# Optimization experiments

Measured on AMD Instinct MI355X. Metric: run time of the kernel, lower is better.

Reference implementation:

```python
import jax, jax.numpy as jnp
import numpy as np

B, D, H, M, N, S = 256, 256, 512, 64, 2048, 3
SHIFTS = (1, 0, -1)  # = range(S//2, -S//2, -1); matches np.roll(eye, s, axis=1) one-hot matrices


def setup_inputs():
    key = jax.random.key(0)
    k = jax.random.split(key, 24)
    f32 = jnp.float32

    def rn(i, shape, scale):
        return jax.random.normal(k[i], shape, f32) * scale

    rh = jax.random.uniform(k[3], (B, N), f32)
    wh = jax.random.uniform(k[4], (B, N), f32)
    sc_ih = 1.0 / np.sqrt(D + M)
    sc_h = 1.0 / np.sqrt(H)
    return dict(
        inp=rn(0, (B, D), 1.0),
        h_tm1=rn(1, (B, H), 0.1),
        c_tm1=rn(2, (B, H), 0.1),
        read_head_tm1=rh / rh.sum(1, keepdims=True),
        write_head_tm1=wh / wh.sum(1, keepdims=True),
        memory=rn(5, (B, N, M), 0.5),
        W_ih=rn(6, (4 * H, D + M), sc_ih), W_hh=rn(7, (4 * H, H), sc_h),
        b_ih=jnp.zeros((4 * H,), f32), b_hh=jnp.zeros((4 * H,), f32),
        W_rk=rn(8, (M, H), sc_h), b_rk=rn(9, (M,), 0.01),
        W_wk=rn(10, (M, H), sc_h), b_wk=rn(11, (M,), 0.01),
        W_rc=rn(12, (3, H), sc_h), b_rc=jnp.zeros((3,), f32),
        W_wc=rn(13, (3, H), sc_h), b_wc=jnp.zeros((3,), f32),
        W_rs=rn(14, (S, H), sc_h), b_rs=jnp.zeros((S,), f32),
        W_ws=rn(15, (S, H), sc_h), b_ws=jnp.zeros((S,), f32),
        W_w=rn(16, (2 * M, H), sc_h), b_w=jnp.zeros((2 * M,), f32),
    )


def _head_params(h, Wk, bk, Wc, bc, Ws, bs):
    kk = jnp.tanh(h @ Wk.T + bk)                     # [B,M] key
    c = h @ Wc.T + bc                                # [B,3]
    beta = jax.nn.relu(c[:, 0:1]) + 1e-4             # focus strength
    g = jax.nn.sigmoid(c[:, 1:2])                    # interpolation gate
    gamma = jax.nn.relu(c[:, 2:3]) + 1.0001          # sharpening power
    s = jax.nn.softmax(h @ Ws.T + bs, axis=1)        # [B,S] shift weights
    return kk, s, beta, g, gamma


def _address(memory, head_tm1, kk, s, beta, g, gamma):
    dot = jnp.einsum('bm,bnm->bn', kk, memory)
    nk = jnp.linalg.norm(kk, axis=1, keepdims=True)  # [B,1]
    nM = jnp.linalg.norm(memory, axis=2)             # [B,N]
    cos = dot / jnp.maximum(nk * nM, 1e-8)
    content = jax.nn.softmax(beta * cos, axis=1)
    inter = g * content + (1.0 - g) * head_tm1       # gated interpolation [B,N]
    # circular shift; identical math to contracting with the one-hot C tensor
    rolled = jnp.stack([jnp.roll(inter, -sh, axis=1) for sh in SHIFTS], axis=1)  # [B,S,N]
    out = jnp.einsum('bsn,bs->bn', rolled, s)
    out = out ** gamma                               # sharpen
    return out / out.sum(1, keepdims=True)


def reference(inp, h_tm1, c_tm1, read_head_tm1, write_head_tm1, memory,
              W_ih, W_hh, b_ih, b_hh, W_rk, b_rk, W_wk, b_wk,
              W_rc, b_rc, W_wc, b_wc, W_rs, b_rs, W_ws, b_ws, W_w, b_w):
    # read addressing uses previous hidden state
    rp = _head_params(h_tm1, W_rk, b_rk, W_rc, b_rc, W_rs, b_rs)
    read_head = _address(memory, read_head_tm1, *rp)
    M_read = jnp.einsum('bn,bnm->bm', read_head, memory)  # [B,M]
    # LSTMCell controller (torch gate order i,f,g,o)
    x = jnp.concatenate([inp, M_read], axis=1)
    z = x @ W_ih.T + b_ih + h_tm1 @ W_hh.T + b_hh
    zi, zf, zg, zo = jnp.split(z, 4, axis=1)
    c_t = jax.nn.sigmoid(zf) * c_tm1 + jax.nn.sigmoid(zi) * jnp.tanh(zg)
    h_t = jax.nn.sigmoid(zo) * jnp.tanh(c_t)
    # write addressing uses new hidden state
    wp = _head_params(h_t, W_wk, b_wk, W_wc, b_wc, W_ws, b_ws)
    write_head = _address(memory, write_head_tm1, *wp)
    wa = h_t @ W_w.T + b_w
    e = jax.nn.sigmoid(wa[:, :M])                    # erase
    a = jnp.tanh(wa[:, M:])                          # add
    ww = write_head[:, :, None]                      # [B,N,1]
    M_out = memory * (1.0 - ww * e[:, None, :]) + ww * a[:, None, :]
    return (h_t, c_t, read_head, write_head, M_out)
```

## Files before the change

kernel.cpp:

```cpp
#include <hip/hip_runtime.h>
#include <hip/hip_bf16.h>

#define Bb 256
#define Hh 512
#define Mm 64
#define Nn 2048

typedef __attribute__((ext_vector_type(8))) short bf16x8;
typedef __attribute__((ext_vector_type(4))) float f32x4;
typedef __attribute__((ext_vector_type(4))) unsigned short u16x4;
typedef __attribute__((ext_vector_type(8))) unsigned short u16x8;

static __device__ __forceinline__ short f2bf(float f) {
    unsigned u = __float_as_uint(f);
    unsigned r = (u + 0x7FFFu + ((u >> 16) & 1u)) >> 16;
    return (short)r;
}
static __device__ __forceinline__ float bf2f(unsigned short u) {
    return __uint_as_float(((unsigned)u) << 16);
}

__global__ __launch_bounds__(256) void convW_headparams_kernel(
    const float* __restrict__ W_ih, const float* __restrict__ W_hh,
    short* __restrict__ Wb,
    const float* __restrict__ h,
    const float* __restrict__ Wk, const float* __restrict__ bk,
    const float* __restrict__ Wc, const float* __restrict__ bc,
    const float* __restrict__ Ws, const float* __restrict__ bs,
    float* __restrict__ kk, float* __restrict__ par)
{
    if (blockIdx.x < 832) {
        unsigned g = blockIdx.x * 256 + threadIdx.x;
        unsigned j = g / 104u;
        unsigned kq = (g - j * 104u) * 8u;
        const float* src = (kq < 320u) ? (W_ih + (size_t)j * 320 + kq)
                                       : (W_hh + (size_t)j * 512 + (kq - 320u));
        float4 a = ((const float4*)src)[0];
        float4 c = ((const float4*)src)[1];
        bf16x8 o;
        o[0] = f2bf(a.x); o[1] = f2bf(a.y); o[2] = f2bf(a.z); o[3] = f2bf(a.w);
        o[4] = f2bf(c.x); o[5] = f2bf(c.y); o[6] = f2bf(c.z); o[7] = f2bf(c.w);
        *(bf16x8*)(Wb + (size_t)j * 832 + kq) = o;
        return;
    }
    int b = blockIdx.x - 832;
    __shared__ float hs[Hh];
    __shared__ float red[6];
    __shared__ float skk[Mm];
    const float* hb = h + (size_t)b * Hh;
    for (int i = threadIdx.x; i < Hh; i += 256) hs[i] = hb[i];
    __syncthreads();
    int m = threadIdx.x >> 2, sub = threadIdx.x & 3;
    {
        const float* w = Wk + (size_t)m * Hh + sub * 128;
        const float* hh = hs + sub * 128;
        float acc = 0.f;
        #pragma unroll 8
        for (int k = 0; k < 128; ++k) acc += hh[k] * w[k];
        acc += __shfl_xor(acc, 1, 64);
        acc += __shfl_xor(acc, 2, 64);
        if (sub == 0) {
            float v = tanhf(acc + bk[m]);
            kk[(size_t)b * Mm + m] = v;
            skk[m] = v;
        }
    }
    if (threadIdx.x < 24) {
        int o = threadIdx.x >> 2, su = threadIdx.x & 3;
        const float* w = ((o < 3) ? (Wc + (size_t)o * Hh) : (Ws + (size_t)(o - 3) * Hh)) + su * 128;
        const float* hh = hs + su * 128;
        float acc = 0.f;
        #pragma unroll 8
        for (int k = 0; k < 128; ++k) acc += hh[k] * w[k];
        acc += __shfl_xor(acc, 1, 64);
        acc += __shfl_xor(acc, 2, 64);
        if (su == 0) red[o] = acc + ((o < 3) ? bc[o] : bs[o - 3]);
    }
    __syncthreads();
    if (threadIdx.x == 0) {
        float beta  = fmaxf(red[0], 0.f) + 1e-4f;
        float g     = 1.f / (1.f + __expf(-red[1]));
        float gamma = fmaxf(red[2], 0.f) + 1.0001f;
        float l0 = red[3], l1 = red[4], l2 = red[5];
        float mx = fmaxf(l0, fmaxf(l1, l2));
        float e0 = __expf(l0 - mx), e1 = __expf(l1 - mx), e2 = __expf(l2 - mx);
        float inv = 1.f / (e0 + e1 + e2);
        float ssq = 0.f;
        #pragma unroll
        for (int i = 0; i < Mm; ++i) ssq += skk[i] * skk[i];
        float* p = par + (size_t)b * 8;
        p[0] = beta; p[1] = g; p[2] = gamma;
        p[3] = e0 * inv; p[4] = e1 * inv; p[5] = e2 * inv;
        p[6] = sqrtf(ssq);
    }
}

__global__ __launch_bounds__(256) void convM_cos_kernel(
    const float* __restrict__ mem, const float* __restrict__ kk,
    const float* __restrict__ par, float* __restrict__ cosv,
    short* __restrict__ memb)
{
    int b  = blockIdx.x >> 3;
    int n0 = (blockIdx.x & 7) << 8;
    int w  = threadIdx.x >> 6;
    int l  = threadIdx.x & 63;
    int m4 = l & 15;
    int rq = l >> 4;

    float4 kv = ((const float4*)(kk + (size_t)b * Mm))[m4];
    float kn = par[(size_t)b * 8 + 6];
    const f32x4* mb4 = (const f32x4*)(mem + (size_t)b * Nn * Mm);
    short* ob = memb + (size_t)b * Nn * Mm;

    #pragma unroll
    for (int q = 0; q < 16; ++q) {
        int n = n0 + w * 64 + q * 4 + rq;
        f32x4 v = __builtin_nontemporal_load(mb4 + (size_t)n * 16 + m4);
        u16x4 o;
        o[0] = (unsigned short)f2bf(v[0]); o[1] = (unsigned short)f2bf(v[1]);
        o[2] = (unsigned short)f2bf(v[2]); o[3] = (unsigned short)f2bf(v[3]);
        *(u16x4*)(ob + (size_t)n * 64 + m4 * 4) = o;
        float dot = v[0] * kv.x + v[1] * kv.y + v[2] * kv.z + v[3] * kv.w;
        float ss  = v[0] * v[0] + v[1] * v[1] + v[2] * v[2] + v[3] * v[3];
        dot += __shfl_xor(dot, 1, 64); ss += __shfl_xor(ss, 1, 64);
        dot += __shfl_xor(dot, 2, 64); ss += __shfl_xor(ss, 2, 64);
        dot += __shfl_xor(dot, 4, 64); ss += __shfl_xor(ss, 4, 64);
        dot += __shfl_xor(dot, 8, 64); ss += __shfl_xor(ss, 8, 64);
        if (m4 == 0) cosv[(size_t)b * Nn + n] = dot / fmaxf(kn * sqrtf(ss), 1e-8f);
    }
}

__global__ __launch_bounds__(1024) void raddr_mread_convA_kernel(
    const float* __restrict__ cosv, const float* __restrict__ par,
    const float* __restrict__ prev, const short* __restrict__ memb,
    const float* __restrict__ inp, const float* __restrict__ h,
    float* __restrict__ outh, short* __restrict__ Ab)
{
    int b = blockIdx.x;
    int t = threadIdx.x;
    int w = t >> 6, l = t & 63;
    __shared__ float csh[Nn];
    __shared__ float redw[16];
    __shared__ float redM[128][8][8];
    __shared__ float mrdL[Mm];

    const float* pv = par + (size_t)b * 8;
    float beta = pv[0], g = pv[1], gamma = pv[2];
    float s0 = pv[3], s1 = pv[4], s2 = pv[5];

    float v0 = beta * cosv[(size_t)b * Nn + t];
    float v1 = beta * cosv[(size_t)b * Nn + t + 1024];
    float mx = fmaxf(v0, v1);
    #pragma unroll
    for (int msk = 1; msk < 64; msk <<= 1) mx = fmaxf(mx, __shfl_xor(mx, msk, 64));
    if (l == 0) redw[w] = mx;
    __syncthreads();
    mx = redw[0];
    #pragma unroll
    for (int i = 1; i < 16; ++i) mx = fmaxf(mx, redw[i]);
    float e0 = __expf(v0 - mx), e1 = __expf(v1 - mx);
    float sum = e0 + e1;
    #pragma unroll
    for (int msk = 1; msk < 64; msk <<= 1) sum += __shfl_xor(sum, msk, 64);
    __syncthreads();
    if (l == 0) redw[w] = sum;
    __syncthreads();
    sum = 0.f;
    #pragma unroll
    for (int i = 0; i < 16; ++i) sum += redw[i];
    float invs = 1.f / sum;
    const float* pb = prev + (size_t)b * Nn;
    float i0 = g * e0 * invs + (1.f - g) * pb[t];
    float i1 = g * e1 * invs + (1.f - g) * pb[t + 1024];
    csh[t] = i0; csh[t + 1024] = i1;
    __syncthreads();
    int n1 = t + 1024;
    float c0 = s0 * csh[(t + 1) & (Nn - 1)] + s1 * i0 + s2 * csh[(t - 1) & (Nn - 1)];
    float c1 = s0 * csh[(n1 + 1) & (Nn - 1)] + s1 * i1 + s2 * csh[(n1 - 1) & (Nn - 1)];
    float p0 = exp2f(gamma * __log2f(c0));
    float p1 = exp2f(gamma * __log2f(c1));
    float osum = p0 + p1;
    #pragma unroll
    for (int msk = 1; msk < 64; msk <<= 1) osum += __shfl_xor(osum, msk, 64);
    __syncthreads();
// ... 24 lines not shown
    }
    #pragma unroll
    for (int j = 0; j < 8; ++j) redM[r][m8][j] = acc[j];
    __syncthreads();
    #pragma unroll
    for (int s = 64; s >= 1; s >>= 1) {
        if (r < s) {
            #pragma unroll
            for (int j = 0; j < 8; ++j) redM[r][m8][j] += redM[r + s][m8][j];
        }
        __syncthreads();
    }
    if (t < 8) {
        #pragma unroll
        for (int j = 0; j < 8; ++j) mrdL[t * 8 + j] = redM[0][t][j];
    }
    __syncthreads();

    if (t < 104) {
        int kq = t * 8;
        float v[8];
        if (kq < 256) {
            const float* s = inp + (size_t)b * 256 + kq;
            #pragma unroll
            for (int i = 0; i < 8; ++i) v[i] = s[i];
        } else if (kq < 320) {
            #pragma unroll
            for (int i = 0; i < 8; ++i) v[i] = mrdL[kq - 256 + i];
        } else {
            const float* s = h + (size_t)b * 512 + (kq - 320);
            #pragma unroll
            for (int i = 0; i < 8; ++i) v[i] = s[i];
        }
        bf16x8 o;
        #pragma unroll
        for (int i = 0; i < 8; ++i) o[i] = f2bf(v[i]);
        *(bf16x8*)(Ab + (size_t)b * 832 + kq) = o;
    }
}

__global__ __launch_bounds__(256) void lstm_gemm_mfma(
    const short* __restrict__ Ab, const short* __restrict__ Wb,
    const float* __restrict__ b_ih, const float* __restrict__ b_hh,
    float* __restrict__ z)
{
    int t = threadIdx.x;
    int r0 = blockIdx.x * 64, c0 = blockIdx.y * 64;
    int w = t >> 6, l = t & 63;
    int wr = (w >> 1) * 32, wc = (w & 1) * 32;
    int lr = l & 15, kb = (l >> 4) * 8;

    const short* A0 = Ab + (size_t)(r0 + wr + lr) * 832 + kb;
    const short* A1 = A0 + 16 * 832;
    const short* B0 = Wb + (size_t)(c0 + wc + lr) * 832 + kb;
    const short* B1 = B0 + 16 * 832;

    f32x4 acc00 = {0.f, 0.f, 0.f, 0.f}, acc01 = {0.f, 0.f, 0.f, 0.f};
    f32x4 acc10 = {0.f, 0.f, 0.f, 0.f}, acc11 = {0.f, 0.f, 0.f, 0.f};

    #pragma unroll 2
    for (int kt = 0; kt < 26; ++kt) {
        int k0 = kt * 32;
        bf16x8 a0 = *(const bf16x8*)(A0 + k0);
        bf16x8 a1 = *(const bf16x8*)(A1 + k0);
        bf16x8 b0 = *(const bf16x8*)(B0 + k0);
        bf16x8 b1 = *(const bf16x8*)(B1 + k0);
        acc00 = __builtin_amdgcn_mfma_f32_16x16x32_bf16(a0, b0, acc00, 0, 0, 0);
        acc01 = __builtin_amdgcn_mfma_f32_16x16x32_bf16(a0, b1, acc01, 0, 0, 0);
        acc10 = __builtin_amdgcn_mfma_f32_16x16x32_bf16(a1, b0, acc10, 0, 0, 0);
        acc11 = __builtin_amdgcn_mfma_f32_16x16x32_bf16(a1, b1, acc11, 0, 0, 0);
    }
    int rq = (l >> 4) * 4;
    #pragma unroll
    for (int q = 0; q < 4; ++q) {
        int row0 = r0 + wr + rq + q;
        int col0 = c0 + wc + lr;
        z[(size_t)row0 * 2048 + col0] = acc00[q] + b_ih[col0] + b_hh[col0];
        z[(size_t)row0 * 2048 + col0 + 16] = acc01[q] + b_ih[col0 + 16] + b_hh[col0 + 16];
        z[(size_t)(row0 + 16) * 2048 + col0] = acc10[q] + b_ih[col0] + b_hh[col0];
        z[(size_t)(row0 + 16) * 2048 + col0 + 16] = acc11[q] + b_ih[col0 + 16] + b_hh[col0 + 16];
    }
}

__global__ __launch_bounds__(1024) void gates_wparams_kernel(
    const float* __restrict__ z, const float* __restrict__ c_tm1,
    const float* __restrict__ Wk, const float* __restrict__ bk,
    const float* __restrict__ Wc, const float* __restrict__ bc,
    const float* __restrict__ Ws, const float* __restrict__ bs,
    const float* __restrict__ W_w, const float* __restrict__ b_w,
    float* __restrict__ h_out, float* __restrict__ c_out,
    float* __restrict__ kk, float* __restrict__ par, float* __restrict__ ea)
{
    int b = blockIdx.x;
    int t = threadIdx.x;
    __shared__ float hs[Hh];
    __shared__ float red6[6];
    __shared__ float skk[Mm];

    if (t < 512) {
        const float* zb = z + (size_t)b * 2048;
        float zi = zb[t], zf = zb[512 + t], zg = zb[1024 + t], zo = zb[1536 + t];
        float si = 1.f / (1.f + __expf(-zi));
        float sf = 1.f / (1.f + __expf(-zf));
        float so = 1.f / (1.f + __expf(-zo));
        float ct = sf * c_tm1[(size_t)b * 512 + t] + si * tanhf(zg);
        float ht = so * tanhf(ct);
        c_out[(size_t)b * 512 + t] = ct;
        h_out[(size_t)b * 512 + t] = ht;
        hs[t] = ht;
    }
    __syncthreads();

    if (t < 256) {
        int m = t >> 2, sub = t & 3;
        const float* w = Wk + (size_t)m * Hh + sub * 128;
        const float* hh = hs + sub * 128;
        float acc = 0.f;
        #pragma unroll 8
        for (int k = 0; k < 128; ++k) acc += hh[k] * w[k];
        acc += __shfl_xor(acc, 1, 64);
        acc += __shfl_xor(acc, 2, 64);
        if (sub == 0) {
            float v = tanhf(acc + bk[m]);
            skk[m] = v;
            kk[(size_t)b * Mm + m] = v;
        }
    } else if (t < 280) {
        int o = (t - 256) >> 2, su = t & 3;
        const float* w = ((o < 3) ? (Wc + (size_t)o * Hh) : (Ws + (size_t)(o - 3) * Hh)) + su * 128;
        const float* hh = hs + su * 128;
        float acc = 0.f;
        #pragma unroll 8
        for (int k = 0; k < 128; ++k) acc += hh[k] * w[k];
        acc += __shfl_xor(acc, 1, 64);
        acc += __shfl_xor(acc, 2, 64);
        if (su == 0) red6[o] = acc + ((o < 3) ? bc[o] : bs[o - 3]);
    } else if (t >= 512) {
        int o = (t - 512) >> 2, su = t & 3;
        const float* w = W_w + (size_t)o * Hh + su * 128;
        const float* hh = hs + su * 128;
        float acc = 0.f;
        #pragma unroll 8
        for (int k = 0; k < 128; ++k) acc += hh[k] * w[k];
        acc += __shfl_xor(acc, 1, 64);
        acc += __shfl_xor(acc, 2, 64);
        if (su == 0) {
            float v = acc + b_w[o];
            ea[(size_t)b * 128 + o] = (o < Mm) ? (1.f / (1.f + __expf(-v))) : tanhf(v);
        }
    }
    __syncthreads();
    if (t < 64) {
        float v = skk[t];
        float ssq = v * v;
        #pragma unroll
        for (int msk = 1; msk < 64; msk <<= 1) ssq += __shfl_xor(ssq, msk, 64);
        if (t == 0) {
            float beta  = fmaxf(red6[0], 0.f) + 1e-4f;
            float g     = 1.f / (1.f + __expf(-red6[1]));
            float gamma = fmaxf(red6[2], 0.f) + 1.0001f;
            float l0 = red6[3], l1 = red6[4], l2 = red6[5];
            float mx = fmaxf(l0, fmaxf(l1, l2));
            float e0 = __expf(l0 - mx), e1 = __expf(l1 - mx), e2 = __expf(l2 - mx);
            float inv = 1.f / (e0 + e1 + e2);
            float* p = par + (size_t)b * 8;
            p[0] = beta; p[1] = g; p[2] = gamma;
            p[3] = e0 * inv; p[4] = e1 * inv; p[5] = e2 * inv;
            p[6] = sqrtf(ssq);
        }
    }
}

__global__ __launch_bounds__(1024) void wfused_kernel(
    const short* __restrict__ memb, const float* __restrict__ kk,
    const float* __restrict__ par, const float* __restrict__ prev,
    float* __restrict__ outh)
{
    int b = blockIdx.x;
    int t = threadIdx.x;
    int w = t >> 6, l = t & 63;
    __shared__ float csh[Nn];
    __shared__ float redw[16];

    const float* pv = par + (size_t)b * 8;
    float kn = pv[6];
    float beta = pv[0], g = pv[1], gamma = pv[2];
    float s0 = pv[3], s1 = pv[4], s2 = pv[5];

    int m8 = l & 7, rg = l >> 3;
    float kv[8];
    {
        const float* kp = kk + (size_t)b * Mm + m8 * 8;
        #pragma unroll
        for (int j = 0; j < 8; ++j) kv[j] = kp[j];
    }
    const short* mb = memb + (size_t)b * Nn * Mm;
    #pragma unroll 4
    for (int it = 0; it < 16; ++it) {
        int n = it * 128 + w * 8 + rg;
        u16x8 uv = *(const u16x8*)(mb + (size_t)n * 64 + m8 * 8);
        float dot = 0.f, ss = 0.f;
        #pragma unroll
        for (int j = 0; j < 8; ++j) {
            float x = bf2f(uv[j]);
            dot += x * kv[j];
            ss  += x * x;
        }
        dot += __shfl_xor(dot, 1, 64); ss += __shfl_xor(ss, 1, 64);
        dot += __shfl_xor(dot, 2, 64); ss += __shfl_xor(ss, 2, 64);
        dot += __shfl_xor(dot, 4, 64); ss += __shfl_xor(ss, 4, 64);
        if (m8 == 0) csh[n] = dot / fmaxf(kn * sqrtf(ss), 1e-8f);
    }
    __syncthreads();

    float v0 = beta * csh[t], v1 = beta * csh[t + 1024];
    float mx = fmaxf(v0, v1);
    #pragma unroll
    for (int msk = 1; msk < 64; msk <<= 1) mx = fmaxf(mx, __shfl_xor(mx, msk, 64));
    if (l == 0) redw[w] = mx;
    __syncthreads();
    mx = redw[0];
    #pragma unroll
    for (int i = 1; i < 16; ++i) mx = fmaxf(mx, redw[i]);
    float e0 = __expf(v0 - mx), e1 = __expf(v1 - mx);
    float sum = e0 + e1;
    #pragma unroll
    for (int msk = 1; msk < 64; msk <<= 1) sum += __shfl_xor(sum, msk, 64);
    __syncthreads();
    if (l == 0) redw[w] = sum;
    __syncthreads();
    sum = 0.f;
    #pragma unroll
    for (int i = 0; i < 16; ++i) sum += redw[i];
    float invs = 1.f / sum;
    const float* pb = prev + (size_t)b * Nn;
    float i0 = g * e0 * invs + (1.f - g) * pb[t];
    float i1 = g * e1 * invs + (1.f - g) * pb[t + 1024];
    __syncthreads();
    csh[t] = i0; csh[t + 1024] = i1;
    __syncthreads();
    int n1 = t + 1024;
    float c0 = s0 * csh[(t + 1) & (Nn - 1)] + s1 * i0 + s2 * csh[(t - 1) & (Nn - 1)];
    float c1 = s0 * csh[(n1 + 1) & (Nn - 1)] + s1 * i1 + s2 * csh[(n1 - 1) & (Nn - 1)];
    float p0 = exp2f(gamma * __log2f(c0));
    float p1 = exp2f(gamma * __log2f(c1));
    float osum = p0 + p1;
    #pragma unroll
    for (int msk = 1; msk < 64; msk <<= 1) osum += __shfl_xor(osum, msk, 64);
    __syncthreads();
    if (l == 0) redw[w] = osum;
    __syncthreads();
    osum = 0.f;
    #pragma unroll
    for (int i = 0; i < 16; ++i) osum += redw[i];
    float inv2 = 1.f / osum;
    outh[(size_t)b * Nn + t] = p0 * inv2;
    outh[(size_t)b * Nn + n1] = p1 * inv2;
}

template <int BF16SRC>
__global__ __launch_bounds__(256) void mout_kernel(
    const float* __restrict__ mem, const short* __restrict__ memb,
    const float* __restrict__ head, const float* __restrict__ ea,
    float* __restrict__ out)
{
    const size_t total8 = (size_t)Bb * Nn * Mm / 8;
    for (size_t i8 = (size_t)blockIdx.x * 256 + threadIdx.x; i8 < total8;
         i8 += (size_t)2048 * 256) {
        size_t row = i8 >> 3;
        int m8 = (int)(i8 & 7);
        int b = (int)(row >> 11);
        float w = head[row];
        float x[8];
        if (BF16SRC) {
            u16x8 uv = __builtin_nontemporal_load((const u16x8*)memb + i8);
            #pragma unroll
            for (int j = 0; j < 8; ++j) x[j] = bf2f(uv[j]);
        } else {
            f32x4 lo = __builtin_nontemporal_load((const f32x4*)mem + i8 * 2);
            f32x4 hi = __builtin_nontemporal_load((const f32x4*)mem + i8 * 2 + 1);
            #pragma unroll
            for (int j = 0; j < 4; ++j) { x[j] = lo[j]; x[4 + j] = hi[j]; }
        }
        const float* ep = ea + (size_t)b * 128 + m8 * 8;
        const float* ap = ep + 64;
        f32x4 o0, o1;
        #pragma unroll
        for (int j = 0; j < 4; ++j) {
            o0[j] = x[j] * (1.f - w * ep[j]) + w * ap[j];
            o1[j] = x[4 + j] * (1.f - w * ep[4 + j]) + w * ap[4 + j];
        }
        __builtin_nontemporal_store(o0, (f32x4*)out + i8 * 2);
        __builtin_nontemporal_store(o1, (f32x4*)out + i8 * 2 + 1);
    }
}

extern "C" void kernel_launch(void* const* d_in, const int* in_sizes, int n_in,
                              void* d_out, int out_size, void* d_ws, size_t ws_size,
                              hipStream_t stream)
{
    const float* inp   = (const float*)d_in[0];
    const float* h_tm1 = (const float*)d_in[1];
    const float* c_tm1 = (const float*)d_in[2];
    const float* rh0   = (const float*)d_in[3];
    const float* wh0   = (const float*)d_in[4];
    const float* mem   = (const float*)d_in[5];
    const float* W_ih  = (const float*)d_in[6];
    const float* W_hh  = (const float*)d_in[7];
    const float* b_ih  = (const float*)d_in[8];
    const float* b_hh  = (const float*)d_in[9];
    const float* W_rk  = (const float*)d_in[10];
    const float* b_rk  = (const float*)d_in[11];
    const float* W_wk  = (const float*)d_in[12];
    const float* b_wk  = (const float*)d_in[13];
    const float* W_rc  = (const float*)d_in[14];
    const float* b_rc  = (const float*)d_in[15];
    const float* W_wc  = (const float*)d_in[16];
    const float* b_wc  = (const float*)d_in[17];
    const float* W_rs  = (const float*)d_in[18];
    const float* b_rs  = (const float*)d_in[19];
    const float* W_ws  = (const float*)d_in[20];
    const float* b_ws  = (const float*)d_in[21];
    const float* W_w   = (const float*)d_in[22];
    const float* b_w   = (const float*)d_in[23];

    float* out   = (float*)d_out;
    float* h_t   = out;
    float* c_t   = out + 131072;
    float* rhead = out + 262144;
    float* whead = out + 786432;
    float* mo    = out + 1310720;
    float* cosbuf = mo;
    float* zbuf   = mo + 524288;
    short* Ab     = (short*)(mo + 1048576);
    short* Wb     = (short*)(mo + 1179648);

    float* ws  = (float*)d_ws;
    float* kk  = ws;
    float* par = ws + 16384;
    float* ea  = ws + 18432;

    const size_t memb_elems = (size_t)Bb * Nn * Mm;
    const bool big_ws = ws_size >= (size_t)51200 * 4 + memb_elems * 2;
    short* memb = big_ws ? (short*)(ws + 51200)
                         : (short*)(mo + 2097152);

    convW_headparams_kernel<<<1088, 256, 0, stream>>>(
        W_ih, W_hh, Wb, h_tm1, W_rk, b_rk, W_rc, b_rc, W_rs, b_rs, kk, par);
    convM_cos_kernel<<<2048, 256, 0, stream>>>(mem, kk, par, cosbuf, memb);
    raddr_mread_convA_kernel<<<Bb, 1024, 0, stream>>>(
        cosbuf, par, rh0, memb, inp, h_tm1, rhead, Ab);
    lstm_gemm_mfma<<<dim3(4, 32), 256, 0, stream>>>(Ab, Wb, b_ih, b_hh, zbuf);
    gates_wparams_kernel<<<Bb, 1024, 0, stream>>>(
        zbuf, c_tm1, W_wk, b_wk, W_wc, b_wc, W_ws, b_ws, W_w, b_w,
        h_t, c_t, kk, par, ea);
    wfused_kernel<<<Bb, 1024, 0, stream>>>(memb, kk, par, wh0, whead);
    if (big_ws)
        mout_kernel<1><<<2048, 256, 0, stream>>>(mem, memb, whead, ea, mo);
    else
        mout_kernel<0><<<2048, 256, 0, stream>>>(mem, memb, whead, ea, mo);
}
```

Measured before the change: 155.6 us.

## Fuse all NTM stages into one cooperative persistent kernel with grid syncs

Replaces the seven-kernel launch sequence with a single cooperative kernel of 256 blocks of 1024 threads, one block per batch row. Stages are separated by three grid.sync calls, and per-batch data (cosine scores, heads, head parameters) stays in shared memory instead of round-tripping through global buffers. This removes launch overhead and intermediate writes. In exchange, the heavy memory-streaming phases now run with only 256 blocks, the LSTM GEMM uses just one block per tile, and the grid barriers add cost. If the cooperative launch fails, the code falls back to the old multi-kernel path.

```diff
diff --git a/kernel.cpp b/kernel.cpp
--- a/kernel.cpp
+++ b/kernel.cpp
@@ -1,5 +1,8 @@
 #include <hip/hip_runtime.h>
 #include <hip/hip_bf16.h>
+#include <hip/hip_cooperative_groups.h>
+
+namespace cg = cooperative_groups;
 
 #define Bb 256
 #define Hh 512
@@ -18,6 +21,431 @@
 }
 static __device__ __forceinline__ float bf2f(unsigned short u) {
     return __uint_as_float(((unsigned)u) << 16);
+}
+
+template <int BF16SRC>
+__global__ __launch_bounds__(1024) void ntm_mega_kernel(
+    const float* __restrict__ inp, const float* __restrict__ h_tm1,
+    const float* __restrict__ c_tm1, const float* __restrict__ rh0,
+    const float* __restrict__ wh0, const float* __restrict__ mem,
+    const float* __restrict__ W_ih, const float* __restrict__ W_hh,
+    const float* __restrict__ b_ih, const float* __restrict__ b_hh,
+    const float* __restrict__ W_rk, const float* __restrict__ b_rk,
+    const float* __restrict__ W_wk, const float* __restrict__ b_wk,
+    const float* __restrict__ W_rc, const float* __restrict__ b_rc,
+    const float* __restrict__ W_wc, const float* __restrict__ b_wc,
+    const float* __restrict__ W_rs, const float* __restrict__ b_rs,
+    const float* __restrict__ W_ws, const float* __restrict__ b_ws,
+    const float* __restrict__ W_w, const float* __restrict__ b_w,
+    float* __restrict__ h_t, float* __restrict__ c_t,
+    float* __restrict__ rhead, float* __restrict__ whead,
+    float* __restrict__ mo, short* __restrict__ Wb, short* __restrict__ Ab,
+    float* __restrict__ zbuf, short* __restrict__ memb)
+{
+    cg::grid_group grid = cg::this_grid();
+    const int b = blockIdx.x;
+    const int t = threadIdx.x;
+    const int w = t >> 6, l = t & 63;
+
+    __shared__ float hs[Hh];
+    __shared__ float red6[6];
+    __shared__ float redw[16];
+    __shared__ float skk[Mm];
+    __shared__ float parL[8];
+    __shared__ float eaL[128];
+    __shared__ float csh[Nn];
+    __shared__ float mrdL[Mm];
+    __shared__ float redM[128][8][8];
+
+    {
+        unsigned g = (unsigned)b * 1024u + (unsigned)t;
+        if (g < 212992u) {
+            unsigned j = g / 104u;
+            unsigned kq = (g - j * 104u) * 8u;
+            const float* src = (kq < 320u) ? (W_ih + (size_t)j * 320 + kq)
+                                           : (W_hh + (size_t)j * 512 + (kq - 320u));
+            f32x4 a = ((const f32x4*)src)[0];
+            f32x4 c = ((const f32x4*)src)[1];
+            bf16x8 o;
+            o[0] = f2bf(a[0]); o[1] = f2bf(a[1]); o[2] = f2bf(a[2]); o[3] = f2bf(a[3]);
+            o[4] = f2bf(c[0]); o[5] = f2bf(c[1]); o[6] = f2bf(c[2]); o[7] = f2bf(c[3]);
+            *(bf16x8*)(Wb + (size_t)j * 832 + kq) = o;
+        }
+    }
+    if (t < Hh) hs[t] = h_tm1[(size_t)b * Hh + t];
+    __syncthreads();
+    if (t < 256) {
+        int m = t >> 2, sub = t & 3;
+        const float* wv = W_rk + (size_t)m * Hh + sub * 128;
+        const float* hh = hs + sub * 128;
+        float acc = 0.f;
+        #pragma unroll 8
+        for (int k = 0; k < 128; ++k) acc += hh[k] * wv[k];
+        acc += __shfl_xor(acc, 1, 64);
+        acc += __shfl_xor(acc, 2, 64);
+        if (sub == 0) skk[m] = tanhf(acc + b_rk[m]);
+    } else if (t < 280) {
+        int o = (t - 256) >> 2, su = t & 3;
+        const float* wv = ((o < 3) ? (W_rc + (size_t)o * Hh) : (W_rs + (size_t)(o - 3) * Hh)) + su * 128;
+        const float* hh = hs + su * 128;
+        float acc = 0.f;
+        #pragma unroll 8
+        for (int k = 0; k < 128; ++k) acc += hh[k] * wv[k];
+        acc += __shfl_xor(acc, 1, 64);
+        acc += __shfl_xor(acc, 2, 64);
+        if (su == 0) red6[o] = acc + ((o < 3) ? b_rc[o] : b_rs[o - 3]);
+    }
+    __syncthreads();
+    if (t < 64) {
+        float v = skk[t];
+        float ssq = v * v;
+        #pragma unroll
+        for (int msk = 1; msk < 64; msk <<= 1) ssq += __shfl_xor(ssq, msk, 64);
+        if (t == 0) {
+            parL[6] = sqrtf(ssq);
+            parL[0] = fmaxf(red6[0], 0.f) + 1e-4f;
+            parL[1] = 1.f / (1.f + __expf(-red6[1]));
+            parL[2] = fmaxf(red6[2], 0.f) + 1.0001f;
+            float l0 = red6[3], l1 = red6[4], l2 = red6[5];
+            float mx = fmaxf(l0, fmaxf(l1, l2));
+            float e0 = __expf(l0 - mx), e1 = __expf(l1 - mx), e2 = __expf(l2 - mx);
+            float inv = 1.f / (e0 + e1 + e2);
+            parL[3] = e0 * inv; parL[4] = e1 * inv; parL[5] = e2 * inv;
+        }
+    }
+    __syncthreads();
+
+    {
+        int m4 = l & 15, rq4 = l >> 4;
+        float4 kv = make_float4(skk[m4 * 4], skk[m4 * 4 + 1], skk[m4 * 4 + 2], skk[m4 * 4 + 3]);
+        float kn = parL[6];
+        const f32x4* mb4 = (const f32x4*)(mem + (size_t)b * Nn * Mm);
+        short* ob = memb + (size_t)b * Nn * Mm;
+        #pragma unroll 4
+        for (int it = 0; it < 32; ++it) {
+            int n = w * 128 + it * 4 + rq4;
+            f32x4 v = __builtin_nontemporal_load(mb4 + (size_t)n * 16 + m4);
+            u16x4 o;
+            o[0] = (unsigned short)f2bf(v[0]); o[1] = (unsigned short)f2bf(v[1]);
+            o[2] = (unsigned short)f2bf(v[2]); o[3] = (unsigned short)f2bf(v[3]);
+            *(u16x4*)(ob + (size_t)n * 64 + m4 * 4) = o;
+            float dot = v[0] * kv.x + v[1] * kv.y + v[2] * kv.z + v[3] * kv.w;
+            float ss  = v[0] * v[0] + v[1] * v[1] + v[2] * v[2] + v[3] * v[3];
+            dot += __shfl_xor(dot, 1, 64); ss += __shfl_xor(ss, 1, 64);
+            dot += __shfl_xor(dot, 2, 64); ss += __shfl_xor(ss, 2, 64);
+            dot += __shfl_xor(dot, 4, 64); ss += __shfl_xor(ss, 4, 64);
+            dot += __shfl_xor(dot, 8, 64); ss += __shfl_xor(ss, 8, 64);
+            if (m4 == 0) csh[n] = dot / fmaxf(kn * sqrtf(ss), 1e-8f);
+        }
+    }
+    __syncthreads();
+
+    {
+        float beta = parL[0], g = parL[1], gamma = parL[2];
+        float s0 = parL[3], s1 = parL[4], s2 = parL[5];
+        float v0 = beta * csh[t], v1 = beta * csh[t + 1024];
+        float mx = fmaxf(v0, v1);
+        #pragma unroll
+        for (int msk = 1; msk < 64; msk <<= 1) mx = fmaxf(mx, __shfl_xor(mx, msk, 64));
+        if (l == 0) redw[w] = mx;
+        __syncthreads();
+        mx = redw[0];
+        #pragma unroll
+        for (int i = 1; i < 16; ++i) mx = fmaxf(mx, redw[i]);
+        float e0 = __expf(v0 - mx), e1 = __expf(v1 - mx);
+        float sum = e0 + e1;
+        #pragma unroll
+        for (int msk = 1; msk < 64; msk <<= 1) sum += __shfl_xor(sum, msk, 64);
+        __syncthreads();
+        if (l == 0) redw[w] = sum;
+        __syncthreads();
+        sum = 0.f;
+        #pragma unroll
+        for (int i = 0; i < 16; ++i) sum += redw[i];
+        float invs = 1.f / sum;
+        const float* pb = rh0 + (size_t)b * Nn;
+        float i0 = g * e0 * invs + (1.f - g) * pb[t];
+        float i1 = g * e1 * invs + (1.f - g) * pb[t + 1024];
+        __syncthreads();
+        csh[t] = i0; csh[t + 1024] = i1;
+        __syncthreads();
+        int n1 = t + 1024;
+        float c0 = s0 * csh[(t + 1) & (Nn - 1)] + s1 * i0 + s2 * csh[(t - 1) & (Nn - 1)];
+        float c1 = s0 * csh[(n1 + 1) & (Nn - 1)] + s1 * i1 + s2 * csh[(n1 - 1) & (Nn - 1)];
+        float p0 = exp2f(gamma * __log2f(c0));
+        float p1 = exp2f(gamma * __log2f(c1));
+        float osum = p0 + p1;
+        #pragma unroll
+        for (int msk = 1; msk < 64; msk <<= 1) osum += __shfl_xor(osum, msk, 64);
+        __syncthreads();
+        if (l == 0) redw[w] = osum;
+        __syncthreads();
+        osum = 0.f;
+        #pragma unroll
+        for (int i = 0; i < 16; ++i) osum += redw[i];
+        float inv2 = 1.f / osum;
+        float h0 = p0 * inv2, h1 = p1 * inv2;
+        rhead[(size_t)b * Nn + t] = h0;
+        rhead[(size_t)b * Nn + n1] = h1;
+        __syncthreads();
+        csh[t] = h0; csh[n1] = h1;
+        __syncthreads();
+    }
+
+    {
+        int m8 = t & 7;
+        int r  = t >> 3;
+        const short* mb = memb + (size_t)b * Nn * Mm;
+        float acc[8] = {};
+        #pragma unroll 4
+        for (int it = 0; it < 16; ++it) {
+            int n = it * 128 + r;
+            float wgt = csh[n];
+            u16x8 uv = *(const u16x8*)(mb + (size_t)n * 64 + m8 * 8);
+            #pragma unroll
+            for (int j = 0; j < 8; ++j) acc[j] += wgt * bf2f(uv[j]);
+        }
+        #pragma unroll
+        for (int j = 0; j < 8; ++j) redM[r][m8][j] = acc[j];
+        __syncthreads();
+        #pragma unroll
+        for (int s = 64; s >= 1; s >>= 1) {
+            if (r < s) {
+                #pragma unroll
+                for (int j = 0; j < 8; ++j) redM[r][m8][j] += redM[r + s][m8][j];
+            }
+            __syncthreads();
+        }
+        if (t < 8) {
+            #pragma unroll
+            for (int j = 0; j < 8; ++j) mrdL[t * 8 + j] = redM[0][t][j];
+        }
+        __syncthreads();
+        if (t < 104) {
+            int kq = t * 8;
+            float v[8];
+            if (kq < 256) {
+                const float* s = inp + (size_t)b * 256 + kq;
+                #pragma unroll
+                for (int i = 0; i < 8; ++i) v[i] = s[i];
+            } else if (kq < 320) {
+                #pragma unroll
+                for (int i = 0; i < 8; ++i) v[i] = mrdL[kq - 256 + i];
+            } else {
+                const float* s = h_tm1 + (size_t)b * 512 + (kq - 320);
+                #pragma unroll
+                for (int i = 0; i < 8; ++i) v[i] = s[i];
+            }
+            bf16x8 o;
+            #pragma unroll
+            for (int i = 0; i < 8; ++i) o[i] = f2bf(v[i]);
+            *(bf16x8*)(Ab + (size_t)b * 832 + kq) = o;
+        }
+    }
+    grid.sync();
+
+    {
+        int row0 = (b & 3) * 64, col0 = (b >> 2) * 32;
+        if (w < 8) {
+            int fr = w & 3, fc = w >> 2;
+            int lr = l & 15, kb = (l >> 4) * 8;
+            const short* A0 = Ab + (size_t)(row0 + fr * 16 + lr) * 832 + kb;
+            const short* B0 = Wb + (size_t)(col0 + fc * 16 + lr) * 832 + kb;
+            f32x4 acc = {0.f, 0.f, 0.f, 0.f};
+            #pragma unroll 2
+            for (int kt = 0; kt < 26; ++kt) {
+                bf16x8 av = *(const bf16x8*)(A0 + kt * 32);
+                bf16x8 bv = *(const bf16x8*)(B0 + kt * 32);
+                acc = __builtin_amdgcn_mfma_f32_16x16x32_bf16(av, bv, acc, 0, 0, 0);
+            }
+            int rq = (l >> 4) * 4;
+            int col = col0 + fc * 16 + lr;
+            float bias = b_ih[col] + b_hh[col];
+            #pragma unroll
+            for (int q = 0; q < 4; ++q)
+                zbuf[(size_t)(row0 + fr * 16 + rq + q) * 2048 + col] = acc[q] + bias;
+        }
+    }
+    grid.sync();
+
+    if (t < 512) {
+        const float* zb = zbuf + (size_t)b * 2048;
+        float zi = zb[t], zf = zb[512 + t], zg = zb[1024 + t], zo = zb[1536 + t];
+        float si = 1.f / (1.f + __expf(-zi));
+        float sf = 1.f / (1.f + __expf(-zf));
+        float so = 1.f / (1.f + __expf(-zo));
+        float ct = sf * c_tm1[(size_t)b * 512 + t] + si * tanhf(zg);
+        float ht = so * tanhf(ct);
+        c_t[(size_t)b * 512 + t] = ct;
+        h_t[(size_t)b * 512 + t] = ht;
+        hs[t] = ht;
+    }
+    __syncthreads();
+    if (t < 256) {
+        int m = t >> 2, sub = t & 3;
+        const float* wv = W_wk + (size_t)m * Hh + sub * 128;
+        const float* hh = hs + sub * 128;
+        float acc = 0.f;
+        #pragma unroll 8
+        for (int k = 0; k < 128; ++k) acc += hh[k] * wv[k];
+        acc += __shfl_xor(acc, 1, 64);
+        acc += __shfl_xor(acc, 2, 64);
+        if (sub == 0) skk[m] = tanhf(acc + b_wk[m]);
+    } else if (t < 280) {
+        int o = (t - 256) >> 2, su = t & 3;
+        const float* wv = ((o < 3) ? (W_wc + (size_t)o * Hh) : (W_ws + (size_t)(o - 3) * Hh)) + su * 128;
+        const float* hh = hs + su * 128;
+        float acc = 0.f;
+        #pragma unroll 8
+        for (int k = 0; k < 128; ++k) acc += hh[k] * wv[k];
+        acc += __shfl_xor(acc, 1, 64);
+        acc += __shfl_xor(acc, 2, 64);
+        if (su == 0) red6[o] = acc + ((o < 3) ? b_wc[o] : b_ws[o - 3]);
+    } else if (t >= 512) {
+        int o = (t - 512) >> 2, su = t & 3;
+        const float* wv = W_w + (size_t)o * Hh + su * 128;
+        const float* hh = hs + su * 128;
+        float acc = 0.f;
+        #pragma unroll 8
+        for (int k = 0; k < 128; ++k) acc += hh[k] * wv[k];
+        acc += __shfl_xor(acc, 1, 64);
+        acc += __shfl_xor(acc, 2, 64);
+        if (su == 0) {
+            float v = acc + b_w[o];
+            eaL[o] = (o < Mm) ? (1.f / (1.f + __expf(-v))) : tanhf(v);
+        }
+    }
+    __syncthreads();
+    if (t < 64) {
+        float v = skk[t];
+        float ssq = v * v;
+        #pragma unroll
+        for (int msk = 1; msk < 64; msk <<= 1) ssq += __shfl_xor(ssq, msk, 64);
+        if (t == 0) {
+            parL[6] = sqrtf(ssq);
+            parL[0] = fmaxf(red6[0], 0.f) + 1e-4f;
+            parL[1] = 1.f / (1.f + __expf(-red6[1]));
+            parL[2] = fmaxf(red6[2], 0.f) + 1.0001f;
+            float l0 = red6[3], l1 = red6[4], l2 = red6[5];
+            float mx = fmaxf(l0, fmaxf(l1, l2));
+            float e0 = __expf(l0 - mx), e1 = __expf(l1 - mx), e2 = __expf(l2 - mx);
+            float inv = 1.f / (e0 + e1 + e2);
+            parL[3] = e0 * inv; parL[4] = e1 * inv; parL[5] = e2 * inv;
+        }
+    }
+    __syncthreads();
+
+    {
+        int m8 = l & 7, rg = l >> 3;
+        float kv8[8];
+        #pragma unroll
+        for (int j = 0; j < 8; ++j) kv8[j] = skk[m8 * 8 + j];
+        float kn = parL[6];
+        const short* mb = memb + (size_t)b * Nn * Mm;
+        #pragma unroll 4
+        for (int it = 0; it < 16; ++it) {
+            int n = it * 128 + w * 8 + rg;
+            u16x8 uv = *(const u16x8*)(mb + (size_t)n * 64 + m8 * 8);
+            float dot = 0.f, ss = 0.f;
+            #pragma unroll
+            for (int j = 0; j < 8; ++j) {
+                float x = bf2f(uv[j]);
+                dot += x * kv8[j];
+                ss  += x * x;
+            }
+            dot += __shfl_xor(dot, 1, 64); ss += __shfl_xor(ss, 1, 64);
+            dot += __shfl_xor(dot, 2, 64); ss += __shfl_xor(ss, 2, 64);
+            dot += __shfl_xor(dot, 4, 64); ss += __shfl_xor(ss, 4, 64);
+            if (m8 == 0) csh[n] = dot / fmaxf(kn * sqrtf(ss), 1e-8f);
+        }
+    }
+    __syncthreads();
+    {
+        float beta = parL[0], g = parL[1], gamma = parL[2];
+        float s0 = parL[3], s1 = parL[4], s2 = parL[5];
+        float v0 = beta * csh[t], v1 = beta * csh[t + 1024];
+        float mx = fmaxf(v0, v1);
+        #pragma unroll
+        for (int msk = 1; msk < 64; msk <<= 1) mx = fmaxf(mx, __shfl_xor(mx, msk, 64));
+        if (l == 0) redw[w] = mx;
+        __syncthreads();
+        mx = redw[0];
+        #pragma unroll
+        for (int i = 1; i < 16; ++i) mx = fmaxf(mx, redw[i]);
+        float e0 = __expf(v0 - mx), e1 = __expf(v1 - mx);
+        float sum = e0 + e1;
+        #pragma unroll
+        for (int msk = 1; msk < 64; msk <<= 1) sum += __shfl_xor(sum, msk, 64);
+        __syncthreads();
+        if (l == 0) redw[w] = sum;
+        __syncthreads();
+        sum = 0.f;
+        #pragma unroll
+        for (int i = 0; i < 16; ++i) sum += redw[i];
+        float invs = 1.f / sum;
+        const float* pb = wh0 + (size_t)b * Nn;
+        float i0 = g * e0 * invs + (1.f - g) * pb[t];
+        float i1 = g * e1 * invs + (1.f - g) * pb[t + 1024];
+        __syncthreads();
+        csh[t] = i0; csh[t + 1024] = i1;
+        __syncthreads();
+        int n1 = t + 1024;
+        float c0 = s0 * csh[(t + 1) & (Nn - 1)] + s1 * i0 + s2 * csh[(t - 1) & (Nn - 1)];
+        float c1 = s0 * csh[(n1 + 1) & (Nn - 1)] + s1 * i1 + s2 * csh[(n1 - 1) & (Nn - 1)];
+        float p0 = exp2f(gamma * __log2f(c0));
+        float p1 = exp2f(gamma * __log2f(c1));
+        float osum = p0 + p1;
+        #pragma unroll
+        for (int msk = 1; msk < 64; msk <<= 1) osum += __shfl_xor(osum, msk, 64);
+        __syncthreads();
+        if (l == 0) redw[w] = osum;
+        __syncthreads();
+        osum = 0.f;
+        #pragma unroll
+        for (int i = 0; i < 16; ++i) osum += redw[i];
+        float inv2 = 1.f / osum;
+        float h0 = p0 * inv2, h1 = p1 * inv2;
+        whead[(size_t)b * Nn + t] = h0;
+        whead[(size_t)b * Nn + t + 1024] = h1;
+        __syncthreads();
+        csh[t] = h0; csh[t + 1024] = h1;
+        __syncthreads();
+    }
+    grid.sync();
+
+    {
+        const short* mb = memb + (size_t)b * Nn * Mm;
+        const float* mf = mem + (size_t)b * Nn * Mm;
+        float* ob = mo + (size_t)b * Nn * Mm;
+        #pragma unroll 4
+        for (int it = 0; it < 16; ++it) {
+            int i8 = it * 1024 + t;
+            int n = i8 >> 3;
+            int m8 = i8 & 7;
+            float wgt = csh[n];
+            float x[8];
+            if (BF16SRC) {
+                u16x8 uv = __builtin_nontemporal_load((const u16x8*)mb + i8);
+                #pragma unroll
+                for (int j = 0; j < 8; ++j) x[j] = bf2f(uv[j]);
+            } else {
+                f32x4 lo = __builtin_nontemporal_load((const f32x4*)mf + i8 * 2);
+                f32x4 hi = __builtin_nontemporal_load((const f32x4*)mf + i8 * 2 + 1);
+                #pragma unroll
+                for (int j = 0; j < 4; ++j) { x[j] = lo[j]; x[4 + j] = hi[j]; }
+            }
+            const float* ep = eaL + m8 * 8;
+            const float* ap = ep + 64;
+            f32x4 o0, o1;
+            #pragma unroll
+            for (int j = 0; j < 4; ++j) {
+                o0[j] = x[j] * (1.f - wgt * ep[j]) + wgt * ap[j];
+                o1[j] = x[4 + j] * (1.f - wgt * ep[4 + j]) + wgt * ap[4 + j];
+            }
+            __builtin_nontemporal_store(o0, (f32x4*)ob + i8 * 2);
+            __builtin_nontemporal_store(o1, (f32x4*)ob + i8 * 2 + 1);
+        }
+    }
 }
 
 __global__ __launch_bounds__(256) void convW_headparams_kernel(
@@ -553,6 +981,27 @@
     short* memb = big_ws ? (short*)(ws + 51200)
                          : (short*)(mo + 2097152);
 
+    {
+        const float *a0 = inp, *a1 = h_tm1, *a2 = c_tm1, *a3 = rh0, *a4 = wh0,
+                    *a5 = mem, *a6 = W_ih, *a7 = W_hh, *a8 = b_ih, *a9 = b_hh,
+                    *a10 = W_rk, *a11 = b_rk, *a12 = W_wk, *a13 = b_wk,
+                    *a14 = W_rc, *a15 = b_rc, *a16 = W_wc, *a17 = b_wc,
+                    *a18 = W_rs, *a19 = b_rs, *a20 = W_ws, *a21 = b_ws,
+                    *a22 = W_w, *a23 = b_w;
+        float *o0 = h_t, *o1 = c_t, *o2 = rhead, *o3 = whead, *o4 = mo, *o7 = zbuf;
+        short *o5 = Wb, *o6 = Ab, *o8 = memb;
+        void* args[] = {
+            &a0, &a1, &a2, &a3, &a4, &a5, &a6, &a7, &a8, &a9,
+            &a10, &a11, &a12, &a13, &a14, &a15, &a16, &a17, &a18, &a19,
+            &a20, &a21, &a22, &a23,
+            &o0, &o1, &o2, &o3, &o4, &o5, &o6, &o7, &o8 };
+        const void* fn = big_ws ? (const void*)&ntm_mega_kernel<1>
+                                : (const void*)&ntm_mega_kernel<0>;
+        hipError_t err = hipLaunchCooperativeKernel(
+            fn, dim3(Bb), dim3(1024), args, 0, stream);
+        if (err == hipSuccess) return;
+    }
+
     convW_headparams_kernel<<<1088, 256, 0, stream>>>(
         W_ih, W_hh, Wb, h_tm1, W_rk, b_rk, W_rc, b_rc, W_rs, b_rs, kk, par);
     convM_cos_kernel<<<2048, 256, 0, stream>>>(mem, kk, par, cosbuf, memb);
```

New measurement: 260.6 us. +67.5%, slower.

## Fuse write addressing into gates kernel and move weight conversion into memory pass

Applied to the files above, without the earlier changes.

The write-head addressing kernel is merged into the LSTM gates kernel, so the write key and head parameters stay in shared memory rather than round-tripping through global memory, and one launch is removed. The bf16 conversion of the LSTM weights moves out of the head-params kernel and is appended as extra blocks to the memory-conversion/cosine kernel. The small head-params kernel then only runs 256 blocks, and the weight conversion overlaps the bandwidth-heavy memory pass. The trade-off is that the fused gates kernel uses more shared memory and is one long serial block per batch row.

```diff
diff --git a/kernel.cpp b/kernel.cpp
--- a/kernel.cpp
+++ b/kernel.cpp
@@ -20,30 +20,14 @@
     return __uint_as_float(((unsigned)u) << 16);
 }
 
-__global__ __launch_bounds__(256) void convW_headparams_kernel(
-    const float* __restrict__ W_ih, const float* __restrict__ W_hh,
-    short* __restrict__ Wb,
+__global__ __launch_bounds__(256) void head_params_kernel(
     const float* __restrict__ h,
     const float* __restrict__ Wk, const float* __restrict__ bk,
     const float* __restrict__ Wc, const float* __restrict__ bc,
     const float* __restrict__ Ws, const float* __restrict__ bs,
     float* __restrict__ kk, float* __restrict__ par)
 {
-    if (blockIdx.x < 832) {
-        unsigned g = blockIdx.x * 256 + threadIdx.x;
-        unsigned j = g / 104u;
-        unsigned kq = (g - j * 104u) * 8u;
-        const float* src = (kq < 320u) ? (W_ih + (size_t)j * 320 + kq)
-                                       : (W_hh + (size_t)j * 512 + (kq - 320u));
-        float4 a = ((const float4*)src)[0];
-        float4 c = ((const float4*)src)[1];
-        bf16x8 o;
-        o[0] = f2bf(a.x); o[1] = f2bf(a.y); o[2] = f2bf(a.z); o[3] = f2bf(a.w);
-        o[4] = f2bf(c.x); o[5] = f2bf(c.y); o[6] = f2bf(c.z); o[7] = f2bf(c.w);
-        *(bf16x8*)(Wb + (size_t)j * 832 + kq) = o;
-        return;
-    }
-    int b = blockIdx.x - 832;
+    int b = blockIdx.x;
     __shared__ float hs[Hh];
     __shared__ float red[6];
     __shared__ float skk[Mm];
@@ -95,11 +79,27 @@
     }
 }
 
-__global__ __launch_bounds__(256) void convM_cos_kernel(
+__global__ __launch_bounds__(256) void convM_cos_convW_kernel(
     const float* __restrict__ mem, const float* __restrict__ kk,
     const float* __restrict__ par, float* __restrict__ cosv,
-    short* __restrict__ memb)
-{
+    short* __restrict__ memb,
+    const float* __restrict__ W_ih, const float* __restrict__ W_hh,
+    short* __restrict__ Wb)
+{
+    if (blockIdx.x >= 2048) {
+        unsigned g = (blockIdx.x - 2048) * 256 + threadIdx.x;
+        unsigned j = g / 104u;
+        unsigned kq = (g - j * 104u) * 8u;
+        const float* src = (kq < 320u) ? (W_ih + (size_t)j * 320 + kq)
+                                       : (W_hh + (size_t)j * 512 + (kq - 320u));
+        float4 a = ((const float4*)src)[0];
+        float4 c = ((const float4*)src)[1];
+        bf16x8 o;
+        o[0] = f2bf(a.x); o[1] = f2bf(a.y); o[2] = f2bf(a.z); o[3] = f2bf(a.w);
+        o[4] = f2bf(c.x); o[5] = f2bf(c.y); o[6] = f2bf(c.z); o[7] = f2bf(c.w);
+        *(bf16x8*)(Wb + (size_t)j * 832 + kq) = o;
+        return;
+    }
     int b  = blockIdx.x >> 3;
     int n0 = (blockIdx.x & 7) << 8;
     int w  = threadIdx.x >> 6;
@@ -290,20 +290,25 @@
     }
 }
 
-__global__ __launch_bounds__(1024) void gates_wparams_kernel(
+__global__ __launch_bounds__(1024) void gates_wfused_kernel(
     const float* __restrict__ z, const float* __restrict__ c_tm1,
     const float* __restrict__ Wk, const float* __restrict__ bk,
     const float* __restrict__ Wc, const float* __restrict__ bc,
     const float* __restrict__ Ws, const float* __restrict__ bs,
     const float* __restrict__ W_w, const float* __restrict__ b_w,
+    const short* __restrict__ memb, const float* __restrict__ prev,
     float* __restrict__ h_out, float* __restrict__ c_out,
-    float* __restrict__ kk, float* __restrict__ par, float* __restrict__ ea)
+    float* __restrict__ ea, float* __restrict__ outh)
 {
     int b = blockIdx.x;
     int t = threadIdx.x;
+    int w = t >> 6, l = t & 63;
     __shared__ float hs[Hh];
     __shared__ float red6[6];
     __shared__ float skk[Mm];
+    __shared__ float parL[8];
+    __shared__ float csh[Nn];
+    __shared__ float redw[16];
 
     if (t < 512) {
         const float* zb = z + (size_t)b * 2048;
@@ -321,35 +326,31 @@
 
     if (t < 256) {
         int m = t >> 2, sub = t & 3;
-        const float* w = Wk + (size_t)m * Hh + sub * 128;
+        const float* wv = Wk + (size_t)m * Hh + sub * 128;
         const float* hh = hs + sub * 128;
         float acc = 0.f;
         #pragma unroll 8
-        for (int k = 0; k < 128; ++k) acc += hh[k] * w[k];
+        for (int k = 0; k < 128; ++k) acc += hh[k] * wv[k];
         acc += __shfl_xor(acc, 1, 64);
         acc += __shfl_xor(acc, 2, 64);
-        if (sub == 0) {
-            float v = tanhf(acc + bk[m]);
-            skk[m] = v;
-            kk[(size_t)b * Mm + m] = v;
-        }
+        if (sub == 0) skk[m] = tanhf(acc + bk[m]);
     } else if (t < 280) {
         int o = (t - 256) >> 2, su = t & 3;
-        const float* w = ((o < 3) ? (Wc + (size_t)o * Hh) : (Ws + (size_t)(o - 3) * Hh)) + su * 128;
+        const float* wv = ((o < 3) ? (Wc + (size_t)o * Hh) : (Ws + (size_t)(o - 3) * Hh)) + su * 128;
         const float* hh = hs + su * 128;
         float acc = 0.f;
         #pragma unroll 8
-        for (int k = 0; k < 128; ++k) acc += hh[k] * w[k];
+        for (int k = 0; k < 128; ++k) acc += hh[k] * wv[k];
         acc += __shfl_xor(acc, 1, 64);
         acc += __shfl_xor(acc, 2, 64);
         if (su == 0) red6[o] = acc + ((o < 3) ? bc[o] : bs[o - 3]);
     } else if (t >= 512) {
         int o = (t - 512) >> 2, su = t & 3;
-        const float* w = W_w + (size_t)o * Hh + su * 128;
+        const float* wv = W_w + (size_t)o * Hh + su * 128;
         const float* hh = hs + su * 128;
         float acc = 0.f;
         #pragma unroll 8
-        for (int k = 0; k < 128; ++k) acc += hh[k] * w[k];
+        for (int k = 0; k < 128; ++k) acc += hh[k] * wv[k];
         acc += __shfl_xor(acc, 1, 64);
         acc += __shfl_xor(acc, 2, 64);
         if (su == 0) {
@@ -364,106 +365,92 @@
         #pragma unroll
         for (int msk = 1; msk < 64; msk <<= 1) ssq += __shfl_xor(ssq, msk, 64);
         if (t == 0) {
-            float beta  = fmaxf(red6[0], 0.f) + 1e-4f;
-            float g     = 1.f / (1.f + __expf(-red6[1]));
-            float gamma = fmaxf(red6[2], 0.f) + 1.0001f;
+            parL[6] = sqrtf(ssq);
+            parL[0] = fmaxf(red6[0], 0.f) + 1e-4f;
+            parL[1] = 1.f / (1.f + __expf(-red6[1]));
+            parL[2] = fmaxf(red6[2], 0.f) + 1.0001f;
             float l0 = red6[3], l1 = red6[4], l2 = red6[5];
             float mx = fmaxf(l0, fmaxf(l1, l2));
             float e0 = __expf(l0 - mx), e1 = __expf(l1 - mx), e2 = __expf(l2 - mx);
             float inv = 1.f / (e0 + e1 + e2);
-            float* p = par + (size_t)b * 8;
-            p[0] = beta; p[1] = g; p[2] = gamma;
-            p[3] = e0 * inv; p[4] = e1 * inv; p[5] = e2 * inv;
-            p[6] = sqrtf(ssq);
-        }
-    }
-}
-
-__global__ __launch_bounds__(1024) void wfused_kernel(
-    const short* __restrict__ memb, const float* __restrict__ kk,
-    const float* __restrict__ par, const float* __restrict__ prev,
-    float* __restrict__ outh)
-{
-    int b = blockIdx.x;
-    int t = threadIdx.x;
-    int w = t >> 6, l = t & 63;
-    __shared__ float csh[Nn];
-    __shared__ float redw[16];
-
-    const float* pv = par + (size_t)b * 8;
-    float kn = pv[6];
-    float beta = pv[0], g = pv[1], gamma = pv[2];
-    float s0 = pv[3], s1 = pv[4], s2 = pv[5];
-
-    int m8 = l & 7, rg = l >> 3;
-    float kv[8];
+            parL[3] = e0 * inv; parL[4] = e1 * inv; parL[5] = e2 * inv;
+        }
+    }
+    __syncthreads();
+
     {
-        const float* kp = kk + (size_t)b * Mm + m8 * 8;
-        #pragma unroll
-        for (int j = 0; j < 8; ++j) kv[j] = kp[j];
-    }
-    const short* mb = memb + (size_t)b * Nn * Mm;
-    #pragma unroll 4
-    for (int it = 0; it < 16; ++it) {
-        int n = it * 128 + w * 8 + rg;
-        u16x8 uv = *(const u16x8*)(mb + (size_t)n * 64 + m8 * 8);
-        float dot = 0.f, ss = 0.f;
-        #pragma unroll
-        for (int j = 0; j < 8; ++j) {
-            float x = bf2f(uv[j]);
-            dot += x * kv[j];
-            ss  += x * x;
-        }
-        dot += __shfl_xor(dot, 1, 64); ss += __shfl_xor(ss, 1, 64);
-        dot += __shfl_xor(dot, 2, 64); ss += __shfl_xor(ss, 2, 64);
-        dot += __shfl_xor(dot, 4, 64); ss += __shfl_xor(ss, 4, 64);
-        if (m8 == 0) csh[n] = dot / fmaxf(kn * sqrtf(ss), 1e-8f);
-    }
-    __syncthreads();
-
-    float v0 = beta * csh[t], v1 = beta * csh[t + 1024];
-    float mx = fmaxf(v0, v1);
-    #pragma unroll
-    for (int msk = 1; msk < 64; msk <<= 1) mx = fmaxf(mx, __shfl_xor(mx, msk, 64));
-    if (l == 0) redw[w] = mx;
-    __syncthreads();
-    mx = redw[0];
-    #pragma unroll
-    for (int i = 1; i < 16; ++i) mx = fmaxf(mx, redw[i]);
-    float e0 = __expf(v0 - mx), e1 = __expf(v1 - mx);
-    float sum = e0 + e1;
-    #pragma unroll
-    for (int msk = 1; msk < 64; msk <<= 1) sum += __shfl_xor(sum, msk, 64);
-    __syncthreads();
-    if (l == 0) redw[w] = sum;
-    __syncthreads();
-    sum = 0.f;
-    #pragma unroll
-    for (int i = 0; i < 16; ++i) sum += redw[i];
-    float invs = 1.f / sum;
-    const float* pb = prev + (size_t)b * Nn;
-    float i0 = g * e0 * invs + (1.f - g) * pb[t];
-    float i1 = g * e1 * invs + (1.f - g) * pb[t + 1024];
-    __syncthreads();
-    csh[t] = i0; csh[t + 1024] = i1;
-    __syncthreads();
-    int n1 = t + 1024;
-    float c0 = s0 * csh[(t + 1) & (Nn - 1)] + s1 * i0 + s2 * csh[(t - 1) & (Nn - 1)];
-    float c1 = s0 * csh[(n1 + 1) & (Nn - 1)] + s1 * i1 + s2 * csh[(n1 - 1) & (Nn - 1)];
-    float p0 = exp2f(gamma * __log2f(c0));
-    float p1 = exp2f(gamma * __log2f(c1));
-    float osum = p0 + p1;
-    #pragma unroll
-    for (int msk = 1; msk < 64; msk <<= 1) osum += __shfl_xor(osum, msk, 64);
-    __syncthreads();
-    if (l == 0) redw[w] = osum;
-    __syncthreads();
-    osum = 0.f;
-    #pragma unroll
-    for (int i = 0; i < 16; ++i) osum += redw[i];
-    float inv2 = 1.f / osum;
-    outh[(size_t)b * Nn + t] = p0 * inv2;
-    outh[(size_t)b * Nn + n1] = p1 * inv2;
+        int m8 = l & 7, rg = l >> 3;
+        float kv8[8];
+        #pragma unroll
+        for (int j = 0; j < 8; ++j) kv8[j] = skk[m8 * 8 + j];
+        float kn = parL[6];
+        const short* mb = memb + (size_t)b * Nn * Mm;
+        #pragma unroll 4
+        for (int it = 0; it < 16; ++it) {
+            int n = it * 128 + w * 8 + rg;
+            u16x8 uv = *(const u16x8*)(mb + (size_t)n * 64 + m8 * 8);
+            float dot = 0.f, ss = 0.f;
+            #pragma unroll
+            for (int j = 0; j < 8; ++j) {
+                float x = bf2f(uv[j]);
+                dot += x * kv8[j];
+                ss  += x * x;
+            }
+            dot += __shfl_xor(dot, 1, 64); ss += __shfl_xor(ss, 1, 64);
+            dot += __shfl_xor(dot, 2, 64); ss += __shfl_xor(ss, 2, 64);
+            dot += __shfl_xor(dot, 4, 64); ss += __shfl_xor(ss, 4, 64);
+            if (m8 == 0) csh[n] = dot / fmaxf(kn * sqrtf(ss), 1e-8f);
+        }
+    }
+    __syncthreads();
+
+    {
+        float beta = parL[0], g = parL[1], gamma = parL[2];
+        float s0 = parL[3], s1 = parL[4], s2 = parL[5];
+        float v0 = beta * csh[t], v1 = beta * csh[t + 1024];
+        float mx = fmaxf(v0, v1);
+        #pragma unroll
+        for (int msk = 1; msk < 64; msk <<= 1) mx = fmaxf(mx, __shfl_xor(mx, msk, 64));
+        if (l == 0) redw[w] = mx;
+        __syncthreads();
+        mx = redw[0];
+        #pragma unroll
+        for (int i = 1; i < 16; ++i) mx = fmaxf(mx, redw[i]);
+        float e0 = __expf(v0 - mx), e1 = __expf(v1 - mx);
+        float sum = e0 + e1;
+        #pragma unroll
+        for (int msk = 1; msk < 64; msk <<= 1) sum += __shfl_xor(sum, msk, 64);
+        __syncthreads();
+        if (l == 0) redw[w] = sum;
+        __syncthreads();
+        sum = 0.f;
+        #pragma unroll
+        for (int i = 0; i < 16; ++i) sum += redw[i];
+        float invs = 1.f / sum;
+        const float* pb = prev + (size_t)b * Nn;
+        float i0 = g * e0 * invs + (1.f - g) * pb[t];
+        float i1 = g * e1 * invs + (1.f - g) * pb[t + 1024];
+        __syncthreads();
+        csh[t] = i0; csh[t + 1024] = i1;
+        __syncthreads();
+        int n1 = t + 1024;
+        float c0 = s0 * csh[(t + 1) & (Nn - 1)] + s1 * i0 + s2 * csh[(t - 1) & (Nn - 1)];
+        float c1 = s0 * csh[(n1 + 1) & (Nn - 1)] + s1 * i1 + s2 * csh[(n1 - 1) & (Nn - 1)];
+        float p0 = exp2f(gamma * __log2f(c0));
+        float p1 = exp2f(gamma * __log2f(c1));
+        float osum = p0 + p1;
+        #pragma unroll
+        for (int msk = 1; msk < 64; msk <<= 1) osum += __shfl_xor(osum, msk, 64);
+        __syncthreads();
+        if (l == 0) redw[w] = osum;
+        __syncthreads();
+        osum = 0.f;
+        #pragma unroll
+        for (int i = 0; i < 16; ++i) osum += redw[i];
+        float inv2 = 1.f / osum;
+        outh[(size_t)b * Nn + t] = p0 * inv2;
+        outh[(size_t)b * Nn + n1] = p1 * inv2;
+    }
 }
 
 template <int BF16SRC>
@@ -553,16 +540,16 @@
     short* memb = big_ws ? (short*)(ws + 51200)
                          : (short*)(mo + 2097152);
 
-    convW_headparams_kernel<<<1088, 256, 0, stream>>>(
-        W_ih, W_hh, Wb, h_tm1, W_rk, b_rk, W_rc, b_rc, W_rs, b_rs, kk, par);
-    convM_cos_kernel<<<2048, 256, 0, stream>>>(mem, kk, par, cosbuf, memb);
+    head_params_kernel<<<Bb, 256, 0, stream>>>(
+        h_tm1, W_rk, b_rk, W_rc, b_rc, W_rs, b_rs, kk, par);
+    convM_cos_convW_kernel<<<2880, 256, 0, stream>>>(
+        mem, kk, par, cosbuf, memb, W_ih, W_hh, Wb);
     raddr_mread_convA_kernel<<<Bb, 1024, 0, stream>>>(
         cosbuf, par, rh0, memb, inp, h_tm1, rhead, Ab);
     lstm_gemm_mfma<<<dim3(4, 32), 256, 0, stream>>>(Ab, Wb, b_ih, b_hh, zbuf);
-    gates_wparams_kernel<<<Bb, 1024, 0, stream>>>(
+    gates_wfused_kernel<<<Bb, 1024, 0, stream>>>(
         zbuf, c_tm1, W_wk, b_wk, W_wc, b_wc, W_ws, b_ws, W_w, b_w,
-        h_t, c_t, kk, par, ea);
-    wfused_kernel<<<Bb, 1024, 0, stream>>>(memb, kk, par, wh0, whead);
+        memb, wh0, h_t, c_t, ea, whead);
     if (big_ws)
         mout_kernel<1><<<2048, 256, 0, stream>>>(mem, memb, whead, ea, mo);
     else
```

Result: no change. 154.0 us (median of 2 runs) (-1.0%).
